# Performance work log

Hardware: AMD Instinct MI355X
Metric: run time of the kernel (lower is better)

Reference implementation:

```python
import jax, jax.numpy as jnp
import numpy as np

B, T, D, H, HD, E, F, K = 512, 32, 512, 16, 32, 4, 2048, 2
EPS = 1e-5

def gelu_gpt2(x):
    c = np.sqrt(2.0 / np.pi).astype(np.float32)
    return 0.5 * x * (1.0 + jnp.tanh(c * (x + 0.044715 * x ** 3)))

def layernorm(x, g, b):
    m = jnp.mean(x, axis=-1, keepdims=True)
    v = jnp.mean((x - m) ** 2, axis=-1, keepdims=True)
    return (x - m) * jax.lax.rsqrt(v + EPS) * g + b

def setup_inputs() -> dict:
    key = jax.random.key(0)
    ks = jax.random.split(key, 12)
    s = 0.02
    return {
        "x": jax.random.normal(ks[0], (B, T, D), jnp.float32),
        "ln1_g": jnp.ones((D,), jnp.float32), "ln1_b": jnp.zeros((D,), jnp.float32),
        "wq": jax.random.normal(ks[1], (H, D, HD), jnp.float32) * s,
        "wk": jax.random.normal(ks[2], (H, D, HD), jnp.float32) * s,
        "wv": jax.random.normal(ks[3], (H, D, HD), jnp.float32) * s,
        "w_proj": jax.random.normal(ks[4], (D, D), jnp.float32) * s,
        "b_proj": jnp.zeros((D,), jnp.float32),
        "ln2_g": jnp.ones((D,), jnp.float32), "ln2_b": jnp.zeros((D,), jnp.float32),
        "w_gate": jax.random.normal(ks[5], (D, E), jnp.float32) * s,
        "w1": jax.random.normal(ks[6], (E, D, F), jnp.float32) * s,
        "b1": jnp.zeros((E, F), jnp.float32),
        "w2": jax.random.normal(ks[7], (E, F, D), jnp.float32) * s,
        "b2": jnp.zeros((E, D), jnp.float32),
    }

def reference(x, ln1_g, ln1_b, wq, wk, wv, w_proj, b_proj, ln2_g, ln2_b, w_gate, w1, b1, w2, b2):
    # --- multi-head causal attention (dropout = eval-mode identity) ---
    h = layernorm(x, ln1_g, ln1_b)                       # [B,T,D]
    q = jnp.einsum('btd,hde->bhte', h, wq)
    k = jnp.einsum('btd,hde->bhte', h, wk)
    v = jnp.einsum('btd,hde->bhte', h, wv)
    # NOTE: original scales by 1/sqrt(n_embd), not head_size
    wei = jnp.einsum('bhte,bhse->bhts', q, k) / jnp.sqrt(jnp.float32(D))
    mask = jnp.tril(jnp.ones((T, T), bool))
    wei = jnp.where(mask, wei, -jnp.inf)
    wei = jax.nn.softmax(wei, axis=-1)
    att = jnp.einsum('bhts,bhse->bhte', wei, v)          # [B,H,T,HD]
    att = att.transpose(0, 2, 1, 3).reshape(B, T, D)     # concat heads
    x = x + att @ w_proj + b_proj
    # --- mixture of experts FFN ---
    h2 = layernorm(x, ln2_g, ln2_b).reshape(-1, D)       # [N,D]
    logits = h2 @ w_gate                                  # [N,E] raw gate output
    # faithful to original: scalar mean over all logits
    ep = jnp.mean(logits)
    bal_loss = ep * jnp.log(ep + 0.1)
    w_top, sel = jax.lax.top_k(logits, K)                # [N,K]
    w_top = jax.nn.softmax(w_top, axis=-1)
    combine = jnp.sum(w_top[:, :, None] * jax.nn.one_hot(sel, E, dtype=x.dtype), axis=1)  # [N,E]
    mid = gelu_gpt2(jnp.einsum('nd,edf->nef', h2, w1) + b1)   # [N,E,F]
    eout = jnp.einsum('nef,efd->ned', mid, w2) + b2           # [N,E,D]
    moe = jnp.einsum('ne,ned->nd', combine, eout).reshape(B, T, D)
    return (x + moe, bal_loss)
```

## Files before the change

kernel.cpp:

```cpp
#include <hip/hip_runtime.h>

typedef unsigned short ushort;
typedef unsigned int   uint;
typedef short bf16x8 __attribute__((ext_vector_type(8)));
typedef float f32x4  __attribute__((ext_vector_type(4)));

__device__ __forceinline__ float bf2f(ushort u){
  union { uint u; float f; } c; c.u = ((uint)u) << 16; return c.f;
}
__device__ __forceinline__ ushort f2bf(float f){
  union { float f; uint u; } c; c.f = f;
  return (ushort)((c.u + 0x7fffu + ((c.u >> 16) & 1u)) >> 16);
}
__device__ __forceinline__ float wredsum(float v){
  #pragma unroll
  for (int off = 32; off > 0; off >>= 1) v += __shfl_xor(v, off);
  return v;
}
__device__ __forceinline__ void gload16(const void* g, void* l){
  __builtin_amdgcn_global_load_lds((__attribute__((address_space(1))) void*)(void*)g,
                                   (__attribute__((address_space(3))) void*)l, 16, 0, 0);
}

template<bool SPLIT>
__global__ __launch_bounds__(256) void transpose_to_bf16(
    const float* __restrict__ src, ushort* __restrict__ dhi, ushort* __restrict__ dlo,
    int R, int C)
{
  __shared__ float tile[32][33];
  size_t zoff = (size_t)blockIdx.z * R * C;
  src += zoff; dhi += zoff; if (SPLIT) dlo += zoff;
  int c0 = blockIdx.x * 32, r0 = blockIdx.y * 32;
  int tx = threadIdx.x & 31, ty = threadIdx.x >> 5;
  #pragma unroll
  for (int i = 0; i < 32; i += 8)
    tile[ty + i][tx] = src[(size_t)(r0 + ty + i) * C + (c0 + tx)];
  __syncthreads();
  #pragma unroll
  for (int i = 0; i < 32; i += 8){
    float v = tile[tx][ty + i];
    ushort hi = f2bf(v);
    dhi[(size_t)(c0 + ty + i) * R + (r0 + tx)] = hi;
    if constexpr (SPLIT)
      dlo[(size_t)(c0 + ty + i) * R + (r0 + tx)] = f2bf(v - bf2f(hi));
  }
}

__global__ __launch_bounds__(256) void transpose_qkv(
    const float* __restrict__ wq, const float* __restrict__ wk, const float* __restrict__ wv,
    ushort* __restrict__ dhi, ushort* __restrict__ dlo)
{
  __shared__ float tile[32][33];
  int z = blockIdx.z;
  int which = z >> 4, h = z & 15;
  const float* src = (which == 0) ? wq : (which == 1) ? wk : wv;
  size_t soff = (size_t)h * 512 * 32;
  size_t doff = (size_t)which * 262144 + soff;
  src += soff;
  int r0 = blockIdx.y * 32;
  int tx = threadIdx.x & 31, ty = threadIdx.x >> 5;
  #pragma unroll
  for (int i = 0; i < 32; i += 8)
    tile[ty + i][tx] = src[(size_t)(r0 + ty + i) * 32 + tx];
  __syncthreads();
  #pragma unroll
  for (int i = 0; i < 32; i += 8){
    float v = tile[tx][ty + i];
    ushort hi = f2bf(v);
    dhi[doff + (size_t)(ty + i) * 512 + (r0 + tx)] = hi;
    dlo[doff + (size_t)(ty + i) * 512 + (r0 + tx)] = f2bf(v - bf2f(hi));
  }
}

__global__ __launch_bounds__(256) void ln_split(
    const float* __restrict__ x, const float* __restrict__ g, const float* __restrict__ b,
    ushort* __restrict__ hhi, ushort* __restrict__ hlo)
{
  int w = threadIdx.x >> 6, lane = threadIdx.x & 63;
  int row = blockIdx.x * 4 + w;
  const float* xr = x + (size_t)row * 512;
  int d = lane * 8;
  float4 a0 = *(const float4*)(xr + d);
  float4 a1 = *(const float4*)(xr + d + 4);
  float v[8] = {a0.x,a0.y,a0.z,a0.w,a1.x,a1.y,a1.z,a1.w};
  float s = 0.f;
  #pragma unroll
  for (int j = 0; j < 8; j++) s += v[j];
  s = wredsum(s);
  float mean = s * (1.f/512.f);
  float q = 0.f;
  #pragma unroll
  for (int j = 0; j < 8; j++){ float t = v[j] - mean; q += t*t; }
  q = wredsum(q);
  float rstd = rsqrtf(q * (1.f/512.f) + 1e-5f);
  ushort hu[8], lu[8];
  #pragma unroll
  for (int j = 0; j < 8; j++){
    float h = (v[j] - mean) * rstd * g[d+j] + b[d+j];
    ushort hi = f2bf(h);
    hu[j] = hi;
    lu[j] = f2bf(h - bf2f(hi));
  }
  uint4 oh, ol;
  oh.x = (uint)hu[0] | ((uint)hu[1]<<16); oh.y = (uint)hu[2] | ((uint)hu[3]<<16);
  oh.z = (uint)hu[4] | ((uint)hu[5]<<16); oh.w = (uint)hu[6] | ((uint)hu[7]<<16);
  ol.x = (uint)lu[0] | ((uint)lu[1]<<16); ol.y = (uint)lu[2] | ((uint)lu[3]<<16);
  ol.z = (uint)lu[4] | ((uint)lu[5]<<16); ol.w = (uint)lu[6] | ((uint)lu[7]<<16);
  *(uint4*)(hhi + (size_t)row*512 + d) = oh;
  *(uint4*)(hlo + (size_t)row*512 + d) = ol;
}

template<int EP>
__global__ __launch_bounds__(256) void gemm_bt(
    const ushort* __restrict__ A, const ushort* __restrict__ Alo,
    const ushort* __restrict__ B, const ushort* __restrict__ Blo,
    int M, int N, int K,
    float* __restrict__ outF,
    const float* __restrict__ bias, const float* __restrict__ resid)
{
  __shared__ __align__(16) ushort As[2][128*32];
  __shared__ __align__(16) ushort Bs[2][128*32];
  const int tid  = threadIdx.x;
  const int lane = tid & 63;
  const int w    = tid >> 6;
  const int wm   = w >> 1, wn = w & 1;
  const int bm   = blockIdx.x, bn = blockIdx.y;

  const int    srow = w*16 + (lane >> 2);
  const int    scol = (lane & 3) * 8;
  const size_t aoff = (size_t)(bm*128 + srow) * K + scol;
  const size_t boff = (size_t)(bn*128 + srow) * K + scol;
  const int lbase0 = (w*16) * 32;
  const int lbase1 = (64 + w*16) * 32;

  f32x4 acc[4][4];
  #pragma unroll
  for (int i = 0; i < 4; i++)
    #pragma unroll
    for (int j = 0; j < 4; j++) acc[i][j] = f32x4{0.f,0.f,0.f,0.f};

  const int nk = K >> 5;
  for (int kt = 0; kt < nk; ++kt) {
    const size_t ko = (size_t)kt * 32;
    gload16(A + aoff + ko,               &As[0][lbase0]);
    gload16(A + aoff + (size_t)64*K + ko,&As[0][lbase1]);
    gload16(B + boff + ko,               &Bs[0][lbase0]);
    gload16(B + boff + (size_t)64*K + ko,&Bs[0][lbase1]);
    gload16(Alo + aoff + ko,               &As[1][lbase0]);
    gload16(Alo + aoff + (size_t)64*K + ko,&As[1][lbase1]);
    gload16(Blo + boff + ko,               &Bs[1][lbase0]);
    gload16(Blo + boff + (size_t)64*K + ko,&Bs[1][lbase1]);
    __syncthreads();

    bf16x8 ah[4], bh[4], al[4], bl[4];
    const int kk = (lane >> 4) * 8;
    const int ar = wm*64 + (lane & 15);
    const int br = wn*64 + (lane & 15);
    #pragma unroll
    for (int i = 0; i < 4; i++){
      ah[i] = *(const bf16x8*)&As[0][(ar + i*16)*32 + kk];
      bh[i] = *(const bf16x8*)&Bs[0][(br + i*16)*32 + kk];
      al[i] = *(const bf16x8*)&As[1][(ar + i*16)*32 + kk];
      bl[i] = *(const bf16x8*)&Bs[1][(br + i*16)*32 + kk];
    }
    #pragma unroll
    for (int i = 0; i < 4; i++)
      #pragma unroll
      for (int j = 0; j < 4; j++){
        acc[i][j] = __builtin_amdgcn_mfma_f32_16x16x32_bf16(ah[i], bh[j], acc[i][j], 0,0,0);
        acc[i][j] = __builtin_amdgcn_mfma_f32_16x16x32_bf16(ah[i], bl[j], acc[i][j], 0,0,0);
        acc[i][j] = __builtin_amdgcn_mfma_f32_16x16x32_bf16(al[i], bh[j], acc[i][j], 0,0,0);
      }
    __syncthreads();
  }

  const int r0 = bm*128 + wm*64;
  const int c0 = bn*128 + wn*64;
  const int cl = lane & 15;
  const int rl = (lane >> 4) * 4;
  #pragma unroll
  for (int i = 0; i < 4; i++){
    #pragma unroll
    for (int r = 0; r < 4; r++){
      const int row = r0 + i*16 + rl + r;
      #pragma unroll
      for (int j = 0; j < 4; j++){
        const int col = c0 + j*16 + cl;
        float v = acc[i][j][r];
        size_t idx = (size_t)row * N + col;
        if constexpr (EP == 0) outF[idx] = v;
        else                   outF[idx] = v + bias[col] + resid[idx];
      }
    }
  }
}

__global__ __launch_bounds__(256) void gemm_w1(
    const ushort* __restrict__ A, const ushort* __restrict__ Ball,
    const float* __restrict__ biasAll, ushort* __restrict__ midOut,
    const int* __restrict__ list, const int* __restrict__ seg)
{
  constexpr int K = 512, N = 2048, NBN = 16;
  __shared__ __align__(16) ushort LB[128*132];
  const int tid = threadIdx.x, lane = tid & 63, w = tid >> 6;
  const int wm = w >> 1, wn = w & 1;

  const int nloc = gridDim.x >> 3;
  const int lid  = (blockIdx.x & 7) * nloc + (blockIdx.x >> 3);
  const int bm   = lid / NBN, bn = lid % NBN;
  if (bm >= seg[4]) return;
  int e = 0;
  while (bm >= seg[e+1]) e++;
  const int ltile = bm - seg[e];
  const int* listE = list + e*16384;

  const int jrows = w * 32;
  const int lrow  = lane >> 3;
  const int lgcol = (((lane & 7) ^ lrow)) * 8;

  size_t asrc[4], bsrc[4];
  const ushort* Bm = Ball + (size_t)e * N * K;
  #pragma unroll
  for (int j = 0; j < 4; j++){
    int ar8 = jrows + j*8 + lrow;
    int tok = listE[ltile*128 + ar8];
    asrc[j] = (size_t)tok * K + lgcol;
    bsrc[j] = (size_t)(bn*128 + ar8) * K + lgcol;
  }

  f32x4 acc[4][4];
  #pragma unroll
  for (int i = 0; i < 4; i++)
    #pragma unroll
    for (int j = 0; j < 4; j++) acc[i][j] = f32x4{0.f,0.f,0.f,0.f};

  const int ar = wm*64 + (lane & 15);
  const int br = wn*64 + (lane & 15);
  const int rsw = lane & 7;

  #pragma unroll
  for (int kt = 0; kt < (K >> 6); ++kt){
    const size_t k0 = (size_t)kt * 64;
    #pragma unroll
    for (int j = 0; j < 4; j++){
      gload16(A  + asrc[j] + k0, &LB[(jrows + j*8)*64]);
      gload16(Bm + bsrc[j] + k0, &LB[8192 + (jrows + j*8)*64]);
    }
    __syncthreads();
    #pragma unroll
    for (int ks = 0; ks < 2; ++ks){
      const int g    = ks*4 + (lane >> 4);
      const int goff = (g ^ rsw) * 8;
      bf16x8 af[4], bfr[4];
      #pragma unroll
      for (int i = 0; i < 4; i++){
        af[i]  = *(const bf16x8*)&LB[(ar + i*16)*64 + goff];
        bfr[i] = *(const bf16x8*)&LB[8192 + (br + i*16)*64 + goff];
      }
      #pragma unroll
      for (int i = 0; i < 4; i++)
        #pragma unroll
        for (int j = 0; j < 4; j++)
          acc[i][j] = __builtin_amdgcn_mfma_f32_16x16x32_bf16(af[i], bfr[j], acc[i][j], 0,0,0);
    }
    __syncthreads();
  }

  const int cl = lane & 15;
  const int rl = (lane >> 4) * 4;
  float bj[4];
  #pragma unroll
  for (int j = 0; j < 4; j++)
    bj[j] = biasAll[e*N + bn*128 + wn*64 + j*16 + cl];
  #pragma unroll
  for (int i = 0; i < 4; i++){
    #pragma unroll
    for (int j = 0; j < 4; j++){
      const int cc = wn*64 + j*16 + cl;
      #pragma unroll
      for (int r = 0; r < 4; r++){
        const int rloc = wm*64 + i*16 + rl + r;
        float t = acc[i][j][r] + bj[j];
        float u2 = 1.5957691216057308f * (t + 0.044715f * t*t*t);
        float ex = __expf(u2);
        float gl = t - t * __builtin_amdgcn_rcpf(ex + 1.f);
        LB[rloc*132 + cc] = f2bf(gl);
      }
    }
  }
  __syncthreads();
  const int ch = tid & 15;
  #pragma unroll
  for (int it = 0; it < 8; ++it){
    const int rr = (tid >> 4) + it*16;
    bf16x8 v = *(const bf16x8*)&LB[rr*132 + ch*8];
    *(bf16x8*)&midOut[(size_t)(bm*128 + rr)*2048 + bn*128 + ch*8] = v;
  }
}

__global__ __launch_bounds__(256) void gemm_w2(
    const ushort* __restrict__ mid, const ushort* __restrict__ Ball,
    const float* __restrict__ biasAll, ushort* __restrict__ eout,
    const int* __restrict__ seg)
{
  constexpr int K = 2048, N = 512, NBN = 4;
  __shared__ __align__(16) ushort LB[128*132];
  const int tid = threadIdx.x, lane = tid & 63, w = tid >> 6;
  const int wm = w >> 1, wn = w & 1;

  const int nloc = gridDim.x >> 3;
  const int lid  = (blockIdx.x & 7) * nloc + (blockIdx.x >> 3);
  const int bm   = lid / NBN, bn = lid % NBN;
  if (bm >= seg[4]) return;
  int e = 0;
  while (bm >= seg[e+1]) e++;

  const int jrows = w * 32;
  const int lrow  = lane >> 3;
  const int lgcol = (((lane & 7) ^ lrow)) * 8;

  size_t asrc[4], bsrc[4];
  const ushort* Bm = Ball + (size_t)e * N * K;
  #pragma unroll
  for (int j = 0; j < 4; j++){
    int ar8 = jrows + j*8 + lrow;
    asrc[j] = (size_t)(bm*128 + ar8) * K + lgcol;
    bsrc[j] = (size_t)(bn*128 + ar8) * K + lgcol;
  }

  f32x4 acc[4][4];
  #pragma unroll
  for (int i = 0; i < 4; i++)
    #pragma unroll
    for (int j = 0; j < 4; j++) acc[i][j] = f32x4{0.f,0.f,0.f,0.f};

  const int ar = wm*64 + (lane & 15);
  const int br = wn*64 + (lane & 15);
  const int rsw = lane & 7;

  for (int kt = 0; kt < (K >> 6); ++kt){
    const size_t k0 = (size_t)kt * 64;
    #pragma unroll
    for (int j = 0; j < 4; j++){
      gload16(mid + asrc[j] + k0, &LB[(jrows + j*8)*64]);
      gload16(Bm  + bsrc[j] + k0, &LB[8192 + (jrows + j*8)*64]);
    }
    __syncthreads();
    #pragma unroll
    for (int ks = 0; ks < 2; ++ks){
      const int g    = ks*4 + (lane >> 4);
      const int goff = (g ^ rsw) * 8;
      bf16x8 af[4], bfr[4];
      #pragma unroll
      for (int i = 0; i < 4; i++){
        af[i]  = *(const bf16x8*)&LB[(ar + i*16)*64 + goff];
        bfr[i] = *(const bf16x8*)&LB[8192 + (br + i*16)*64 + goff];
      }
      #pragma unroll
      for (int i = 0; i < 4; i++)
        #pragma unroll
        for (int j = 0; j < 4; j++)
          acc[i][j] = __builtin_amdgcn_mfma_f32_16x16x32_bf16(af[i], bfr[j], acc[i][j], 0,0,0);
    }
    __syncthreads();
  }

  const int cl = lane & 15;
  const int rl = (lane >> 4) * 4;
  float bj[4];
  #pragma unroll
  for (int j = 0; j < 4; j++)
    bj[j] = biasAll[e*N + bn*128 + wn*64 + j*16 + cl];
  #pragma unroll
  for (int i = 0; i < 4; i++){
    #pragma unroll
    for (int j = 0; j < 4; j++){
      const int cc = wn*64 + j*16 + cl;
      #pragma unroll
      for (int r = 0; r < 4; r++){
        const int rloc = wm*64 + i*16 + rl + r;
        LB[rloc*132 + cc] = f2bf(acc[i][j][r] + bj[j]);
      }
    }
  }
  __syncthreads();
  const int ch = tid & 15;
  #pragma unroll
  for (int it = 0; it < 8; ++it){
    const int rr = (tid >> 4) + it*16;
    bf16x8 v = *(const bf16x8*)&LB[rr*132 + ch*8];
    *(bf16x8*)&eout[(size_t)(bm*128 + rr)*512 + bn*128 + ch*8] = v;
  }
}

__global__ __launch_bounds__(256) void moe_combine(
    const ushort* __restrict__ eout, const int2* __restrict__ rowSlots,
    const float2* __restrict__ wts, float* __restrict__ out)
{
  int w = threadIdx.x >> 6, lane = threadIdx.x & 63;
  int row = blockIdx.x * 4 + w;
  int2 rs = rowSlots[row];
  float2 wv = wts[row];
  int d = lane * 8;
  uint4 u0 = *(const uint4*)(eout + (size_t)rs.x*512 + d);
  uint4 u1 = *(const uint4*)(eout + (size_t)rs.y*512 + d);
  float* op = out + (size_t)row*512 + d;
  float4 o0 = *(float4*)op;
  float4 o1 = *(float4*)(op + 4);
  o0.x += wv.x*bf2f((ushort)u0.x)        + wv.y*bf2f((ushort)u1.x);
  o0.y += wv.x*bf2f((ushort)(u0.x>>16))  + wv.y*bf2f((ushort)(u1.x>>16));
  o0.z += wv.x*bf2f((ushort)u0.y)        + wv.y*bf2f((ushort)u1.y);
  o0.w += wv.x*bf2f((ushort)(u0.y>>16))  + wv.y*bf2f((ushort)(u1.y>>16));
  o1.x += wv.x*bf2f((ushort)u0.z)        + wv.y*bf2f((ushort)u1.z);
  o1.y += wv.x*bf2f((ushort)(u0.z>>16))  + wv.y*bf2f((ushort)(u1.z>>16));
  o1.z += wv.x*bf2f((ushort)u0.w)        + wv.y*bf2f((ushort)u1.w);
  o1.w += wv.x*bf2f((ushort)(u0.w>>16))  + wv.y*bf2f((ushort)(u1.w>>16));
  *(float4*)op       = o0;
  *(float4*)(op + 4) = o1;
}

__global__ __launch_bounds__(64) void attn32(
    const float* __restrict__ qkv, ushort* __restrict__ atthi, ushort* __restrict__ attlo)
{
  int bh = blockIdx.x; int b = bh >> 4, h = bh & 15;
  __shared__ float qs[32][33], ks[32][33], vs[32][33], ps[32][33];
  int lane = threadIdx.x;
  int t = lane >> 1, cb = (lane & 1) * 16;
  const float* src = qkv + (size_t)(b*32 + t)*1536 + h*32 + cb;
  #pragma unroll
  for (int j = 0; j < 16; j += 4){
    float4 q4 = *(const float4*)(src + j);
    float4 k4 = *(const float4*)(src + 512 + j);
    float4 v4 = *(const float4*)(src + 1024 + j);
    qs[t][cb+j]=q4.x; qs[t][cb+j+1]=q4.y; qs[t][cb+j+2]=q4.z; qs[t][cb+j+3]=q4.w;
    ks[t][cb+j]=k4.x; ks[t][cb+j+1]=k4.y; ks[t][cb+j+2]=k4.z; ks[t][cb+j+3]=k4.w;
    vs[t][cb+j]=v4.x; vs[t][cb+j+1]=v4.y; vs[t][cb+j+2]=v4.z; vs[t][cb+j+3]=v4.w;
  }
  __syncthreads();
  const float scale = 0.044194173824159216f;
  float sc[16];
  #pragma unroll
  for (int j = 0; j < 16; j++){
    int c = cb + j;
    if (c <= t) {
      float d = 0.f;
      #pragma unroll
      for (int i = 0; i < 32; i++) d += qs[t][i] * ks[c][i];
      sc[j] = d * scale;
    } else sc[j] = -1e30f;
  }
  float mx = -1e30f;
  #pragma unroll
  for (int j = 0; j < 16; j++) mx = fmaxf(mx, sc[j]);
  mx = fmaxf(mx, __shfl_xor(mx, 1));
  float p[16], sum = 0.f;
  #pragma unroll
  for (int j = 0; j < 16; j++){
    int c = cb + j;
    if (c <= t) { p[j] = expf(sc[j] - mx); sum += p[j]; } else p[j] = 0.f;
  }
  sum += __shfl_xor(sum, 1);
  float inv = 1.f / sum;
  #pragma unroll
  for (int j = 0; j < 16; j++) ps[t][cb+j] = p[j] * inv;
  __syncthreads();
  float o[16];
  #pragma unroll
  for (int j = 0; j < 16; j++) o[j] = 0.f;
  for (int s2 = 0; s2 <= t; ++s2){
    float wv = ps[t][s2];
    #pragma unroll
    for (int j = 0; j < 16; j++) o[j] += wv * vs[s2][cb+j];
  }
  size_t base = (size_t)(b*32 + t)*512 + h*32 + cb;
  ushort hu[16], lu[16];
  #pragma unroll
  for (int j = 0; j < 16; j++){
    ushort hi = f2bf(o[j]);
    hu[j] = hi; lu[j] = f2bf(o[j] - bf2f(hi));
  }
  uint4 oh0, oh1, ol0, ol1;
  oh0.x=(uint)hu[0]|((uint)hu[1]<<16);  oh0.y=(uint)hu[2]|((uint)hu[3]<<16);
  oh0.z=(uint)hu[4]|((uint)hu[5]<<16);  oh0.w=(uint)hu[6]|((uint)hu[7]<<16);
  oh1.x=(uint)hu[8]|((uint)hu[9]<<16);  oh1.y=(uint)hu[10]|((uint)hu[11]<<16);
  oh1.z=(uint)hu[12]|((uint)hu[13]<<16);oh1.w=(uint)hu[14]|((uint)hu[15]<<16);
  ol0.x=(uint)lu[0]|((uint)lu[1]<<16);  ol0.y=(uint)lu[2]|((uint)lu[3]<<16);
  ol0.z=(uint)lu[4]|((uint)lu[5]<<16);  ol0.w=(uint)lu[6]|((uint)lu[7]<<16);
  ol1.x=(uint)lu[8]|((uint)lu[9]<<16);  ol1.y=(uint)lu[10]|((uint)lu[11]<<16);
  ol1.z=(uint)lu[12]|((uint)lu[13]<<16);ol1.w=(uint)lu[14]|((uint)lu[15]<<16);
  *(uint4*)(atthi + base)     = oh0;  *(uint4*)(atthi + base + 8) = oh1;
  *(uint4*)(attlo + base)     = ol0;  *(uint4*)(attlo + base + 8) = ol1;
}

__global__ __launch_bounds__(256) void ln2_gate(
    const float* __restrict__ x1, const float* __restrict__ g, const float* __restrict__ b,
    const float* __restrict__ wgate, ushort* __restrict__ h2,
    int* __restrict__ selp, float2* __restrict__ wts,
    int* __restrict__ blockCnt, float* __restrict__ partials)
{
  __shared__ float wsumLds[4];
  __shared__ int   selLds[4];
  int w = threadIdx.x >> 6, lane = threadIdx.x & 63;
  int row = blockIdx.x * 4 + w;
  const float* xr = x1 + (size_t)row * 512;
  int d = lane * 8;
  float4 a0 = *(const float4*)(xr + d);
  float4 a1 = *(const float4*)(xr + d + 4);
  float v[8] = {a0.x,a0.y,a0.z,a0.w,a1.x,a1.y,a1.z,a1.w};
  float s = 0.f;
  #pragma unroll
  for (int j = 0; j < 8; j++) s += v[j];
  s = wredsum(s);
  float mean = s * (1.f/512.f);
  float q = 0.f;
  #pragma unroll
  for (int j = 0; j < 8; j++){ float t = v[j] - mean; q += t*t; }
  q = wredsum(q);
  float rstd = rsqrtf(q * (1.f/512.f) + 1e-5f);
  float acc0=0.f, acc1=0.f, acc2=0.f, acc3=0.f;
  ushort hu[8];
  #pragma unroll
  for (int j = 0; j < 8; j++){
    float h = (v[j] - mean) * rstd * g[d+j] + b[d+j];
    hu[j] = f2bf(h);
    float4 wgv = *(const float4*)(wgate + (size_t)(d+j)*4);
    acc0 += h * wgv.x; acc1 += h * wgv.y; acc2 += h * wgv.z; acc3 += h * wgv.w;
  }
  uint4 oh;
  oh.x=(uint)hu[0]|((uint)hu[1]<<16); oh.y=(uint)hu[2]|((uint)hu[3]<<16);
  oh.z=(uint)hu[4]|((uint)hu[5]<<16); oh.w=(uint)hu[6]|((uint)hu[7]<<16);
  *(uint4*)(h2 + (size_t)row*512 + d) = oh;
  acc0 = wredsum(acc0); acc1 = wredsum(acc1); acc2 = wredsum(acc2); acc3 = wredsum(acc3);
  if (lane == 0){
    float l[4] = {acc0, acc1, acc2, acc3};
    int i0 = 0;
    for (int e = 1; e < 4; e++) if (l[e] > l[i0]) i0 = e;
    int i1 = -1;
    for (int e = 0; e < 4; e++){ if (e == i0) continue; if (i1 < 0 || l[e] > l[i1]) i1 = e; }
    float e1 = expf(l[i1] - l[i0]);
    float w1v = e1 / (1.f + e1), w0v = 1.f / (1.f + e1);
    int packed = i0 | (i1 << 8);
    selp[row] = packed;
    wts[row]  = make_float2(w0v, w1v);
    selLds[w] = packed;
    wsumLds[w] = l[0] + l[1] + l[2] + l[3];
  }
  __syncthreads();
  if (threadIdx.x < 4){
    int e = threadIdx.x, c = 0;
    #pragma unroll
    for (int i = 0; i < 4; i++){
      int sp = selLds[i];
      c += ((sp & 0xff) == e) + (((sp >> 8) & 0xff) == e);
    }
    blockCnt[e*4096 + blockIdx.x] = c;
  }
  if (threadIdx.x == 0)
    partials[blockIdx.x] = wsumLds[0] + wsumLds[1] + wsumLds[2] + wsumLds[3];
}

__global__ __launch_bounds__(256) void scan_offsets(
    const int* __restrict__ blockCnt, int* __restrict__ blockOff,
    int* __restrict__ cnt, int* __restrict__ seg,
    const float* __restrict__ partials, float* __restrict__ lossOut)
{
  __shared__ int cntL[4];
  __shared__ float ws4[4];
  int w = threadIdx.x >> 6, lane = threadIdx.x & 63;
  const int* src = blockCnt + w*4096;
  int* dst = blockOff + w*4096;
  int off = 0;
  for (int i = 0; i < 4096; i += 64){
    int v = src[i + lane];
    int orig = v;
    #pragma unroll
    for (int dlt = 1; dlt < 64; dlt <<= 1){
      int t = __shfl_up(v, dlt);
      if (lane >= dlt) v += t;
    }
    dst[i + lane] = off + v - orig;
    off += __shfl(v, 63);
  }
  if (lane == 0){ cnt[w] = off; cntL[w] = off; }
  __syncthreads();
  if (threadIdx.x == 0){
    int t = 0;
    for (int e = 0; e < 4; e++){ seg[e] = t; t += (cntL[e] + 127) >> 7; }
    seg[4] = t;
  }
  float s = 0.f;
  for (int i = threadIdx.x; i < 4096; i += 256) s += partials[i];
  s = wredsum(s);
  if ((threadIdx.x & 63) == 0) ws4[threadIdx.x >> 6] = s;
  __syncthreads();
  if (threadIdx.x == 0){
    float tot = ws4[0] + ws4[1] + ws4[2] + ws4[3];
    float ep = tot * (1.f/65536.f);
    lossOut[0] = ep * logf(ep + 0.1f);
  }
}

__global__ __launch_bounds__(256) void route_write(
    const int* __restrict__ selp, const int* __restrict__ blockOff,
    const int* __restrict__ seg, int* __restrict__ list, int2* __restrict__ rowSlots)
{
  int row = blockIdx.x * 256 + threadIdx.x;
  int g = row & ~3;
  int b = row >> 2;
  int my = selp[row];
  int e0 = my & 0xff, e1 = (my >> 8) & 0xff;
  int r0 = 0, r1 = 0;
  for (int r = g; r < row; ++r){
    int sp = selp[r];
    int a = sp & 0xff, c = (sp >> 8) & 0xff;
    r0 += (a == e0) + (c == e0);
    r1 += (a == e1) + (c == e1);
  }
  int slot0 = blockOff[e0*4096 + b] + r0;
  int slot1 = blockOff[e1*4096 + b] + r1;
  list[e0*16384 + slot0] = row;
  list[e1*16384 + slot1] = row;
  rowSlots[row] = make_int2(seg[e0]*128 + slot0, seg[e1]*128 + slot1);
}

extern "C" void kernel_launch(void* const* d_in, const int* in_sizes, int n_in,
                              void* d_out, int out_size, void* d_ws, size_t ws_size,
                              hipStream_t stream)
{
  const float* x     = (const float*)d_in[0];
  const float* ln1g  = (const float*)d_in[1];
  const float* ln1b  = (const float*)d_in[2];
  const float* wq    = (const float*)d_in[3];
  const float* wk    = (const float*)d_in[4];
  const float* wv    = (const float*)d_in[5];
  const float* wproj = (const float*)d_in[6];
  const float* bproj = (const float*)d_in[7];
  const float* ln2g  = (const float*)d_in[8];
  const float* ln2b  = (const float*)d_in[9];
  const float* wgate = (const float*)d_in[10];
  const float* w1    = (const float*)d_in[11];
  const float* b1    = (const float*)d_in[12];
  const float* w2    = (const float*)d_in[13];
  const float* b2    = (const float*)d_in[14];
  float* out = (float*)d_out;

  char* ws = (char*)d_ws;
  ushort* hHi   = (ushort*)(ws + 0);
  ushort* hLo   = (ushort*)(ws + 16777216);
  ushort* qkvTh = (ushort*)(ws + 33554432);
  ushort* qkvTl = (ushort*)(ws + 35127296);
  ushort* pTh   = (ushort*)(ws + 36700160);
  ushort* pTl   = (ushort*)(ws + 37224448);
  float*  qkvF  = (float*)(ws + 37748736);
  ushort* attHi = (ushort*)(ws + 138412032);
  ushort* attLo = (ushort*)(ws + 155189248);
  ushort* mid   = (ushort*)(ws + 0);
  ushort* eout  = (ushort*)(ws + 137183744);
  ushort* h2    = (ushort*)(ws + 171966464);
  ushort* w1T   = (ushort*)(ws + 188743680);
  ushort* w2T   = (ushort*)(ws + 197132288);
  char* rb = ws + 136314880;
  int*    cnt      = (int*)   (rb + 0);
  int*    seg      = (int*)   (rb + 256);
  int*    list     = (int*)   (rb + 512);
  int2*   rowSlots = (int2*)  (rb + 262656);
  float*  partials = (float*) (rb + 524800);
  int*    selp     = (int*)   (rb + 541184);
  float2* wts      = (float2*)(rb + 606720);
  int*    blockCnt = (int*)   (rb + 737792);
  int*    blockOff = (int*)   (rb + 803328);

  transpose_qkv<<<dim3(1,16,48), 256, 0, stream>>>(wq, wk, wv, qkvTh, qkvTl);
  transpose_to_bf16<true ><<<dim3(16,16,1), 256, 0, stream>>>(wproj, pTh, pTl, 512, 512);
  transpose_to_bf16<false><<<dim3(64,16,4), 256, 0, stream>>>(w1, w1T, nullptr, 512, 2048);
  transpose_to_bf16<false><<<dim3(16,64,4), 256, 0, stream>>>(w2, w2T, nullptr, 2048, 512);

  ln_split<<<dim3(4096), 256, 0, stream>>>(x, ln1g, ln1b, hHi, hLo);

  gemm_bt<0><<<dim3(128,12), 256, 0, stream>>>(hHi, hLo, qkvTh, qkvTl,
      16384, 1536, 512, qkvF, nullptr, nullptr);

  attn32<<<dim3(8192), 64, 0, stream>>>(qkvF, attHi, attLo);

  gemm_bt<1><<<dim3(128,4), 256, 0, stream>>>(attHi, attLo, pTh, pTl,
      16384, 512, 512, out, bproj, x);

  (void)hipMemsetAsync(list, 0, 4*16384*sizeof(int), stream);
  ln2_gate<<<dim3(4096), 256, 0, stream>>>(out, ln2g, ln2b, wgate, h2, selp, wts, blockCnt, partials);
  scan_offsets<<<dim3(1), 256, 0, stream>>>(blockCnt, blockOff, cnt, seg, partials, out + 8388608);
  route_write<<<dim3(64), 256, 0, stream>>>(selp, blockOff, seg, list, rowSlots);

  gemm_w1<<<dim3(4160), 256, 0, stream>>>(h2,  w1T, b1, mid,  list, seg);
  gemm_w2<<<dim3(1040), 256, 0, stream>>>(mid, w2T, b2, eout, seg);
  moe_combine<<<dim3(4096), 256, 0, stream>>>(eout, rowSlots, wts, out);
}
```

Before: 486.9 us.

## Double-buffer LDS and shrink M-tile to 64 in MoE expert GEMMs

Both expert GEMMs (w1 and w2) now use 64x128 output tiles instead of 128x128, doubling the grid and cutting per-block accumulator registers. The shared-memory staging is double-buffered so the next K-slice's global-to-LDS loads are issued before the MFMAs on the current slice. This aims to hide global load latency and reduce padding waste on ragged per-expert tile counts. In exchange, B-tile data is reloaded by twice as many blocks and each MFMA step has a lower compute-to-load ratio.

```diff
diff --git a/kernel.cpp b/kernel.cpp
--- a/kernel.cpp
+++ b/kernel.cpp
@@ -201,64 +201,79 @@
     const int* __restrict__ list, const int* __restrict__ seg)
 {
   constexpr int K = 512, N = 2048, NBN = 16;
-  __shared__ __align__(16) ushort LB[128*132];
+  __shared__ __align__(16) ushort LB[24576];
   const int tid = threadIdx.x, lane = tid & 63, w = tid >> 6;
   const int wm = w >> 1, wn = w & 1;
 
   const int nloc = gridDim.x >> 3;
   const int lid  = (blockIdx.x & 7) * nloc + (blockIdx.x >> 3);
   const int bm   = lid / NBN, bn = lid % NBN;
-  if (bm >= seg[4]) return;
+  if (bm >= seg[4] * 2) return;
   int e = 0;
-  while (bm >= seg[e+1]) e++;
-  const int ltile = bm - seg[e];
+  while (bm >= seg[e+1] * 2) e++;
+  const int t64 = bm - seg[e] * 2;
   const int* listE = list + e*16384;
 
-  const int jrows = w * 32;
   const int lrow  = lane >> 3;
-  const int lgcol = (((lane & 7) ^ lrow)) * 8;
-
-  size_t asrc[4], bsrc[4];
+  const int lgcol = ((lane & 7) ^ lrow) * 8;
+
+  size_t asrc[2];
+  #pragma unroll
+  for (int j = 0; j < 2; j++){
+    int ar8 = w*16 + j*8 + lrow;
+    int tok = listE[t64*64 + ar8];
+    asrc[j] = (size_t)tok * K + lgcol;
+  }
+  size_t bsrc[4];
   const ushort* Bm = Ball + (size_t)e * N * K;
   #pragma unroll
   for (int j = 0; j < 4; j++){
-    int ar8 = jrows + j*8 + lrow;
-    int tok = listE[ltile*128 + ar8];
-    asrc[j] = (size_t)tok * K + lgcol;
-    bsrc[j] = (size_t)(bn*128 + ar8) * K + lgcol;
-  }
-
-  f32x4 acc[4][4];
-  #pragma unroll
-  for (int i = 0; i < 4; i++)
+    int br8 = w*32 + j*8 + lrow;
+    bsrc[j] = (size_t)(bn*128 + br8) * K + lgcol;
+  }
+
+  f32x4 acc[2][4];
+  #pragma unroll
+  for (int i = 0; i < 2; i++)
     #pragma unroll
     for (int j = 0; j < 4; j++) acc[i][j] = f32x4{0.f,0.f,0.f,0.f};
 
-  const int ar = wm*64 + (lane & 15);
+  constexpr int nk = K >> 6;
+
+  #pragma unroll
+  for (int j = 0; j < 2; j++) gload16(A  + asrc[j], &LB[(w*16 + j*8)*64]);
+  #pragma unroll
+  for (int j = 0; j < 4; j++) gload16(Bm + bsrc[j], &LB[8192 + (w*32 + j*8)*64]);
+  __syncthreads();
+
+  const int ar = wm*32 + (lane & 15);
   const int br = wn*64 + (lane & 15);
   const int rsw = lane & 7;
 
-  #pragma unroll
-  for (int kt = 0; kt < (K >> 6); ++kt){
-    const size_t k0 = (size_t)kt * 64;
-    #pragma unroll
-    for (int j = 0; j < 4; j++){
-      gload16(A  + asrc[j] + k0, &LB[(jrows + j*8)*64]);
-      gload16(Bm + bsrc[j] + k0, &LB[8192 + (jrows + j*8)*64]);
-    }
-    __syncthreads();
+  for (int kt = 0; kt < nk; ++kt){
+    const int cur  = kt & 1;
+    const int curA = cur * 4096;
+    const int curB = 8192 + cur * 8192;
+    if (kt + 1 < nk){
+      const int nxtA = (cur ^ 1) * 4096;
+      const int nxtB = 8192 + (cur ^ 1) * 8192;
+      const size_t k0 = (size_t)(kt + 1) * 64;
+      #pragma unroll
+      for (int j = 0; j < 2; j++) gload16(A  + asrc[j] + k0, &LB[nxtA + (w*16 + j*8)*64]);
+      #pragma unroll
+      for (int j = 0; j < 4; j++) gload16(Bm + bsrc[j] + k0, &LB[nxtB + (w*32 + j*8)*64]);
+    }
     #pragma unroll
     for (int ks = 0; ks < 2; ++ks){
       const int g    = ks*4 + (lane >> 4);
       const int goff = (g ^ rsw) * 8;
-      bf16x8 af[4], bfr[4];
-      #pragma unroll
-      for (int i = 0; i < 4; i++){
-        af[i]  = *(const bf16x8*)&LB[(ar + i*16)*64 + goff];
-        bfr[i] = *(const bf16x8*)&LB[8192 + (br + i*16)*64 + goff];
-      }
-      #pragma unroll
-      for (int i = 0; i < 4; i++)
+      bf16x8 af[2], bfr[4];
+      #pragma unroll
+      for (int i = 0; i < 2; i++) af[i]  = *(const bf16x8*)&LB[curA + (ar + i*16)*64 + goff];
+      #pragma unroll
+      for (int j = 0; j < 4; j++) bfr[j] = *(const bf16x8*)&LB[curB + (br + j*16)*64 + goff];
+      #pragma unroll
+      for (int i = 0; i < 2; i++)
         #pragma unroll
         for (int j = 0; j < 4; j++)
           acc[i][j] = __builtin_amdgcn_mfma_f32_16x16x32_bf16(af[i], bfr[j], acc[i][j], 0,0,0);
@@ -273,13 +288,13 @@
   for (int j = 0; j < 4; j++)
     bj[j] = biasAll[e*N + bn*128 + wn*64 + j*16 + cl];
   #pragma unroll
-  for (int i = 0; i < 4; i++){
+  for (int i = 0; i < 2; i++){
     #pragma unroll
     for (int j = 0; j < 4; j++){
       const int cc = wn*64 + j*16 + cl;
       #pragma unroll
       for (int r = 0; r < 4; r++){
-        const int rloc = wm*64 + i*16 + rl + r;
+        const int rloc = wm*32 + i*16 + rl + r;
         float t = acc[i][j][r] + bj[j];
         float u2 = 1.5957691216057308f * (t + 0.044715f * t*t*t);
         float ex = __expf(u2);
@@ -291,10 +306,10 @@
   __syncthreads();
   const int ch = tid & 15;
   #pragma unroll
-  for (int it = 0; it < 8; ++it){
+  for (int it = 0; it < 4; ++it){
     const int rr = (tid >> 4) + it*16;
     bf16x8 v = *(const bf16x8*)&LB[rr*132 + ch*8];
-    *(bf16x8*)&midOut[(size_t)(bm*128 + rr)*2048 + bn*128 + ch*8] = v;
+    *(bf16x8*)&midOut[(size_t)(bm*64 + rr)*2048 + bn*128 + ch*8] = v;
   }
 }
 
@@ -304,60 +319,76 @@
     const int* __restrict__ seg)
 {
   constexpr int K = 2048, N = 512, NBN = 4;
-  __shared__ __align__(16) ushort LB[128*132];
+  __shared__ __align__(16) ushort LB[24576];
   const int tid = threadIdx.x, lane = tid & 63, w = tid >> 6;
   const int wm = w >> 1, wn = w & 1;
 
   const int nloc = gridDim.x >> 3;
   const int lid  = (blockIdx.x & 7) * nloc + (blockIdx.x >> 3);
   const int bm   = lid / NBN, bn = lid % NBN;
-  if (bm >= seg[4]) return;
+  if (bm >= seg[4] * 2) return;
   int e = 0;
-  while (bm >= seg[e+1]) e++;
-
-  const int jrows = w * 32;
+  while (bm >= seg[e+1] * 2) e++;
+
   const int lrow  = lane >> 3;
-  const int lgcol = (((lane & 7) ^ lrow)) * 8;
-
-  size_t asrc[4], bsrc[4];
+  const int lgcol = ((lane & 7) ^ lrow) * 8;
+
+  size_t asrc[2];
+  #pragma unroll
+  for (int j = 0; j < 2; j++){
+    int ar8 = w*16 + j*8 + lrow;
+    asrc[j] = (size_t)(bm*64 + ar8) * K + lgcol;
+  }
+  size_t bsrc[4];
   const ushort* Bm = Ball + (size_t)e * N * K;
   #pragma unroll
   for (int j = 0; j < 4; j++){
-    int ar8 = jrows + j*8 + lrow;
-    asrc[j] = (size_t)(bm*128 + ar8) * K + lgcol;
-    bsrc[j] = (size_t)(bn*128 + ar8) * K + lgcol;
-  }
-
-  f32x4 acc[4][4];
-  #pragma unroll
-  for (int i = 0; i < 4; i++)
+    int br8 = w*32 + j*8 + lrow;
+    bsrc[j] = (size_t)(bn*128 + br8) * K + lgcol;
+  }
+
+  f32x4 acc[2][4];
+  #pragma unroll
+  for (int i = 0; i < 2; i++)
     #pragma unroll
     for (int j = 0; j < 4; j++) acc[i][j] = f32x4{0.f,0.f,0.f,0.f};
 
-  const int ar = wm*64 + (lane & 15);
+  constexpr int nk = K >> 6;
+
+  #pragma unroll
+  for (int j = 0; j < 2; j++) gload16(mid + asrc[j], &LB[(w*16 + j*8)*64]);
+  #pragma unroll
+  for (int j = 0; j < 4; j++) gload16(Bm  + bsrc[j], &LB[8192 + (w*32 + j*8)*64]);
+  __syncthreads();
+
+  const int ar = wm*32 + (lane & 15);
   const int br = wn*64 + (lane & 15);
   const int rsw = lane & 7;
 
-  for (int kt = 0; kt < (K >> 6); ++kt){
-    const size_t k0 = (size_t)kt * 64;
-    #pragma unroll
-    for (int j = 0; j < 4; j++){
-      gload16(mid + asrc[j] + k0, &LB[(jrows + j*8)*64]);
-      gload16(Bm  + bsrc[j] + k0, &LB[8192 + (jrows + j*8)*64]);
-    }
-    __syncthreads();
+  for (int kt = 0; kt < nk; ++kt){
+    const int cur  = kt & 1;
+    const int curA = cur * 4096;
+    const int curB = 8192 + cur * 8192;
+    if (kt + 1 < nk){
+      const int nxtA = (cur ^ 1) * 4096;
+      const int nxtB = 8192 + (cur ^ 1) * 8192;
+      const size_t k0 = (size_t)(kt + 1) * 64;
+      #pragma unroll
+      for (int j = 0; j < 2; j++) gload16(mid + asrc[j] + k0, &LB[nxtA + (w*16 + j*8)*64]);
+      #pragma unroll
+      for (int j = 0; j < 4; j++) gload16(Bm  + bsrc[j] + k0, &LB[nxtB + (w*32 + j*8)*64]);
+    }
     #pragma unroll
     for (int ks = 0; ks < 2; ++ks){
       const int g    = ks*4 + (lane >> 4);
       const int goff = (g ^ rsw) * 8;
-      bf16x8 af[4], bfr[4];
-      #pragma unroll
-      for (int i = 0; i < 4; i++){
-        af[i]  = *(const bf16x8*)&LB[(ar + i*16)*64 + goff];
-        bfr[i] = *(const bf16x8*)&LB[8192 + (br + i*16)*64 + goff];
-      }
-      #pragma unroll
-      for (int i = 0; i < 4; i++)
+      bf16x8 af[2], bfr[4];
+      #pragma unroll
+      for (int i = 0; i < 2; i++) af[i]  = *(const bf16x8*)&LB[curA + (ar + i*16)*64 + goff];
+      #pragma unroll
+      for (int j = 0; j < 4; j++) bfr[j] = *(const bf16x8*)&LB[curB + (br + j*16)*64 + goff];
+      #pragma unroll
+      for (int i = 0; i < 2; i++)
         #pragma unroll
         for (int j = 0; j < 4; j++)
           acc[i][j] = __builtin_amdgcn_mfma_f32_16x16x32_bf16(af[i], bfr[j], acc[i][j], 0,0,0);
@@ -372,13 +403,13 @@
   for (int j = 0; j < 4; j++)
     bj[j] = biasAll[e*N + bn*128 + wn*64 + j*16 + cl];
   #pragma unroll
-  for (int i = 0; i < 4; i++){
+  for (int i = 0; i < 2; i++){
     #pragma unroll
     for (int j = 0; j < 4; j++){
       const int cc = wn*64 + j*16 + cl;
       #pragma unroll
       for (int r = 0; r < 4; r++){
-        const int rloc = wm*64 + i*16 + rl + r;
+        const int rloc = wm*32 + i*16 + rl + r;
         LB[rloc*132 + cc] = f2bf(acc[i][j][r] + bj[j]);
       }
     }
@@ -386,10 +417,10 @@
   __syncthreads();
   const int ch = tid & 15;
   #pragma unroll
-  for (int it = 0; it < 8; ++it){
+  for (int it = 0; it < 4; ++it){
     const int rr = (tid >> 4) + it*16;
     bf16x8 v = *(const bf16x8*)&LB[rr*132 + ch*8];
-    *(bf16x8*)&eout[(size_t)(bm*128 + rr)*512 + bn*128 + ch*8] = v;
+    *(bf16x8*)&eout[(size_t)(bm*64 + rr)*512 + bn*128 + ch*8] = v;
   }
 }
 
@@ -690,7 +721,7 @@
   scan_offsets<<<dim3(1), 256, 0, stream>>>(blockCnt, blockOff, cnt, seg, partials, out + 8388608);
   route_write<<<dim3(64), 256, 0, stream>>>(selp, blockOff, seg, list, rowSlots);
 
-  gemm_w1<<<dim3(4160), 256, 0, stream>>>(h2,  w1T, b1, mid,  list, seg);
-  gemm_w2<<<dim3(1040), 256, 0, stream>>>(mid, w2T, b2, eout, seg);
+  gemm_w1<<<dim3(8320), 256, 0, stream>>>(h2,  w1T, b1, mid,  list, seg);
+  gemm_w2<<<dim3(2080), 256, 0, stream>>>(mid, w2T, b2, eout, seg);
   moe_combine<<<dim3(4096), 256, 0, stream>>>(eout, rowSlots, wts, out);
 }
```

Result: faster. 466.2 us (-4.3%).
